# Performance work log

Hardware: AMD Instinct MI355X
Metric: run time of the kernel (lower is better)

The kernel has to match this reference:

```python
import jax, jax.numpy as jnp
import numpy as np

H = 8      # n_heads
DK = 64    # d_k per head
EPS = 1e-5       # InstanceNorm1d eps
SLOPE = 0.01     # LeakyReLU negative slope


def setup_inputs() -> dict:
    key = jax.random.key(0)
    ks = jax.random.split(key, 6)
    B, C, L = 16, 256, 1024
    HD = H * DK  # 512
    return {
        "x": jax.random.normal(ks[0], (B, C, L), dtype=jnp.float32),
        "Wq": jax.random.normal(ks[1], (HD, C), dtype=jnp.float32) * 0.02,
        "Wk": jax.random.normal(ks[2], (HD, C), dtype=jnp.float32) * 0.02,
        "Wv": jax.random.normal(ks[3], (HD, C), dtype=jnp.float32) * 0.02,
        "Wo": jax.random.normal(ks[4], (C, HD), dtype=jnp.float32) * 0.02,
        "gamma": jax.random.normal(ks[5], (1,), dtype=jnp.float32),
    }


def reference(x, Wq, Wk, Wv, Wo, gamma):
    B, C, L = x.shape
    # conv1x1 projections (bias=False) == channel matmuls -> [B, H*DK, L]
    # then reshape/permute into heads: [B, H, L, DK]
    def proj(W):
        y = jnp.einsum('oc,bcl->bol', W, x)          # [B, H*DK, L]
        return y.reshape(B, H, DK, L).transpose(0, 1, 3, 2)  # [B, H, L, DK]

    q, k, v = proj(Wq), proj(Wk), proj(Wv)
    # softmax-free linear attention: (Q K^T / d_k) V
    logits = jnp.einsum('bhld,bhmd->bhlm', q, k) / DK  # [B, H, L, L]
    out = jnp.einsum('bhlm,bhmd->bhld', logits, v)     # [B, H, L, DK]
    # merge heads back to channel-first [B, H*DK, L]
    merged = out.transpose(0, 1, 3, 2).reshape(B, H * DK, L)
    # output conv1x1 -> [B, C, L]
    o = jnp.einsum('oc,bcl->bol', Wo, merged)
    # InstanceNorm1d (affine=False): normalize over L per (b, c)
    mu = jnp.mean(o, axis=-1, keepdims=True)
    var = jnp.var(o, axis=-1, keepdims=True)
    o = (o - mu) * jax.lax.rsqrt(var + EPS)
    # gamma-scaled residual + LeakyReLU
    y = o * gamma + x
    return jnp.where(y >= 0, y, SLOPE * y)
```

## Files before the change

### kernel.cpp

```cpp
#include <hip/hip_runtime.h>

typedef __bf16 bf16;
typedef bf16 bf16x8 __attribute__((ext_vector_type(8)));
typedef bf16 bf16x4 __attribute__((ext_vector_type(4)));
typedef float f32x4 __attribute__((ext_vector_type(4)));

#define EPS 1e-5f
#define SLOPE 0.01f

__device__ __forceinline__ void gld_lds16(const bf16* g, bf16* l) {
    __builtin_amdgcn_global_load_lds(
        (const __attribute__((address_space(1))) unsigned int*)g,
        (__attribute__((address_space(3))) unsigned int*)l, 16, 0, 0);
}

__global__ __launch_bounds__(256) void prep_kernel(
    const float* __restrict__ x,
    const float* __restrict__ Wq, const float* __restrict__ Wk,
    const float* __restrict__ Wv, const float* __restrict__ Wo,
    bf16* __restrict__ xT, bf16* __restrict__ xB,
    bf16* __restrict__ WkB, bf16* __restrict__ WvB,
    bf16* __restrict__ WoB, bf16* __restrict__ WqT)
{
    __shared__ float tile[64][65];
    const int id = blockIdx.x;
    const int t = threadIdx.x;
    if (id < 1024) {
        const int lt = id & 15, ct = (id >> 4) & 3, b = id >> 6;
        {
            const int cl = t >> 2;
            const int l4 = (t & 3) << 4;
            const float* src = x + (size_t)(b * 256 + ct * 64 + cl) * 1024 + lt * 64 + l4;
            float4 v0 = ((const float4*)src)[0];
            float4 v1 = ((const float4*)src)[1];
            float4 v2 = ((const float4*)src)[2];
            float4 v3 = ((const float4*)src)[3];
            bf16x8 r0, r1;
            r0[0]=(bf16)v0.x; r0[1]=(bf16)v0.y; r0[2]=(bf16)v0.z; r0[3]=(bf16)v0.w;
            r0[4]=(bf16)v1.x; r0[5]=(bf16)v1.y; r0[6]=(bf16)v1.z; r0[7]=(bf16)v1.w;
            r1[0]=(bf16)v2.x; r1[1]=(bf16)v2.y; r1[2]=(bf16)v2.z; r1[3]=(bf16)v2.w;
            r1[4]=(bf16)v3.x; r1[5]=(bf16)v3.y; r1[6]=(bf16)v3.z; r1[7]=(bf16)v3.w;
            bf16* xbd = xB + (size_t)(b * 256 + ct * 64 + cl) * 1024 + lt * 64 + l4;
            *(bf16x8*)xbd = r0;
            *(bf16x8*)(xbd + 8) = r1;
            float* tr = &tile[cl][l4];
            tr[0]=v0.x; tr[1]=v0.y; tr[2]=v0.z; tr[3]=v0.w;
            tr[4]=v1.x; tr[5]=v1.y; tr[6]=v1.z; tr[7]=v1.w;
            tr[8]=v2.x; tr[9]=v2.y; tr[10]=v2.z; tr[11]=v2.w;
            tr[12]=v3.x; tr[13]=v3.y; tr[14]=v3.z; tr[15]=v3.w;
        }
        __syncthreads();
        {
            const int lw = t >> 2;
            const int ec = (t & 3) << 4;
            bf16x8 o0, o1;
            #pragma unroll
            for (int ii = 0; ii < 8; ++ii) {
                o0[ii] = (bf16)tile[ec + ii][lw];
                o1[ii] = (bf16)tile[ec + 8 + ii][lw];
            }
            bf16* dst = xT + (size_t)(b * 1024 + lt * 64 + lw) * 256 + ct * 64 + ec;
            *(bf16x8*)dst = o0;
            *(bf16x8*)(dst + 8) = o1;
        }
    } else if (id < 1408) {
        const int i = (id - 1024) * 1024 + t * 4;
        const float* src; bf16* dst;
        if (i < 131072)      { src = Wk + i;            dst = WkB + i; }
        else if (i < 262144) { src = Wv + (i - 131072); dst = WvB + (i - 131072); }
        else                 { src = Wo + (i - 262144); dst = WoB + (i - 262144); }
        float4 v = *(const float4*)src;
        bf16x4 o;
        o[0]=(bf16)v.x; o[1]=(bf16)v.y; o[2]=(bf16)v.z; o[3]=(bf16)v.w;
        *(bf16x4*)dst = o;
    } else {
        const int id2 = id - 1408;
        const int h = id2 >> 2, ct = id2 & 3;
        {
            const int e  = t >> 2;
            const int c4 = (t & 3) << 4;
            const float* src = Wq + (size_t)(h * 64 + e) * 256 + ct * 64 + c4;
            float4 v0 = ((const float4*)src)[0];
            float4 v1 = ((const float4*)src)[1];
            float4 v2 = ((const float4*)src)[2];
            float4 v3 = ((const float4*)src)[3];
            float* tr = &tile[e][c4];
            tr[0]=v0.x; tr[1]=v0.y; tr[2]=v0.z; tr[3]=v0.w;
            tr[4]=v1.x; tr[5]=v1.y; tr[6]=v1.z; tr[7]=v1.w;
            tr[8]=v2.x; tr[9]=v2.y; tr[10]=v2.z; tr[11]=v2.w;
            tr[12]=v3.x; tr[13]=v3.y; tr[14]=v3.z; tr[15]=v3.w;
        }
        __syncthreads();
        {
            const int c  = t >> 2;
            const int e4 = (t & 3) << 4;
            bf16x8 o0, o1;
            #pragma unroll
            for (int ii = 0; ii < 8; ++ii) {
                o0[ii] = (bf16)tile[e4 + ii][c];
                o1[ii] = (bf16)tile[e4 + 8 + ii][c];
            }
            bf16* dst = WqT + (size_t)h * 16384 + (size_t)(ct * 64 + c) * 64 + e4;
            *(bf16x8*)dst = o0;
            *(bf16x8*)(dst + 8) = o1;
        }
    }
}

template<int KDIM, typename OutT>
__global__ __launch_bounds__(256) void gemm128_bt(
    const bf16* __restrict__ A, const bf16* __restrict__ Bt, OutT* __restrict__ C,
    long long sA, long long sBt, long long sC, int ldC)
{
    __shared__ bf16 As[128 * 32];
    __shared__ bf16 Bs[128 * 32];
    const int z = blockIdx.z;
    A  += (size_t)z * sA;
    Bt += (size_t)z * sBt;
    C  += (size_t)z * sC;
    const int m0 = blockIdx.x * 128;
    const int n0 = blockIdx.y * 128;
    const int t = threadIdx.x, w = t >> 6, l = t & 63;
    const int srow = w * 16 + (l >> 2);
    const int ske  = (l & 3) * 8;
    const bf16* ga = A  + (size_t)(m0 + srow) * KDIM + ske;
    const bf16* gb = Bt + (size_t)(n0 + srow) * KDIM + ske;
    bf16* la = As + srow * 32 + ske;
    bf16* lb = Bs + srow * 32 + ske;
    const int lm = l & 15, lq = l >> 4;
    const int wm = (w & 1) * 64, wn = (w >> 1) * 64;

    f32x4 acc[4][4] = {};
    for (int kt = 0; kt < KDIM / 32; ++kt) {
        const int k0 = kt * 32;
        gld_lds16(ga + k0, la);
        gld_lds16(ga + k0 + (size_t)64 * KDIM, la + 64 * 32);
        gld_lds16(gb + k0, lb);
        gld_lds16(gb + k0 + (size_t)64 * KDIM, lb + 64 * 32);
        __syncthreads();
        bf16x8 af[4], bfr[4];
        #pragma unroll
        for (int i = 0; i < 4; ++i)
            af[i] = *(const bf16x8*)(As + (wm + i * 16 + lm) * 32 + lq * 8);
        #pragma unroll
        for (int j = 0; j < 4; ++j)
            bfr[j] = *(const bf16x8*)(Bs + (wn + j * 16 + lm) * 32 + lq * 8);
        #pragma unroll
        for (int i = 0; i < 4; ++i)
            #pragma unroll
            for (int j = 0; j < 4; ++j)
                acc[i][j] = __builtin_amdgcn_mfma_f32_16x16x32_bf16(af[i], bfr[j], acc[i][j], 0, 0, 0);
        __syncthreads();
    }
    #pragma unroll
    for (int i = 0; i < 4; ++i)
        #pragma unroll
        for (int j = 0; j < 4; ++j) {
            const int row = m0 + wm + i * 16 + lq * 4;
            const int col = n0 + wn + j * 16 + lm;
            OutT* cp = C + (size_t)row * ldC + col;
            #pragma unroll
            for (int r = 0; r < 4; ++r)
                cp[(size_t)r * ldC] = (OutT)acc[i][j][r];
        }
}

__global__ __launch_bounds__(256) void chain_kernel(
    const bf16* __restrict__ G, const bf16* __restrict__ WvB,
    const bf16* __restrict__ WkB, const bf16* __restrict__ WqT,
    bf16* __restrict__ WmT)
{
    __shared__ __align__(16) bf16 bufA[64 * 256];
    __shared__ __align__(16) bf16 bufB[256 * 64];
    __shared__ __align__(16) bf16 Ss[64 * 256];
    __shared__ __align__(16) bf16 Tb[64 * 64];

    const int bh = blockIdx.x;
    const int b = bh >> 3, h = bh & 7;
    const int t = threadIdx.x, w = t >> 6, l = t & 63;
    const int lm = l & 15, lq = l >> 4;

    #pragma unroll
    for (int it = 0; it < 8; ++it) {
        const int slot = it * 256 + t;
        const int d = slot >> 5, seg = slot & 31;
        const int kq = (seg & 24) | ((seg & 7) ^ (d & 7));
        gld_lds16(WvB + (size_t)(h * 64 + d) * 256 + kq * 8, bufA + slot * 8);
    }
    f32x4 accS[4][4] = {};
    for (int ck = 0; ck < 4; ++ck) {
        #pragma unroll
        for (int it = 0; it < 8; ++it) {
            const int slot = it * 256 + t;
            const int cp = slot >> 3, seg = slot & 7;
            const int kq = seg ^ (cp & 7);
            gld_lds16(G + (size_t)b * 65536 + (size_t)cp * 256 + ck * 64 + kq * 8,
                      bufB + slot * 8);
        }
        __syncthreads();
        #pragma unroll
        for (int kt = 0; kt < 2; ++kt) {
            bf16x8 af[4], bfr[4];
            #pragma unroll
            for (int mf = 0; mf < 4; ++mf) {
                const int m = mf * 16 + lm;
                const int kqg = ck * 8 + kt * 4 + lq;
                const int seg = (kqg & 24) | ((kqg & 7) ^ (m & 7));
                af[mf] = *(const bf16x8*)(bufA + m * 256 + seg * 8);
            }
            #pragma unroll
            for (int nf = 0; nf < 4; ++nf) {
                const int n = w * 64 + nf * 16 + lm;
                const int kq = kt * 4 + lq;
                const int seg = kq ^ (n & 7);
                bfr[nf] = *(const bf16x8*)(bufB + n * 64 + seg * 8);
            }
            #pragma unroll
            for (int mf = 0; mf < 4; ++mf)
                #pragma unroll
                for (int nf = 0; nf < 4; ++nf)
                    accS[mf][nf] = __builtin_amdgcn_mfma_f32_16x16x32_bf16(
                        af[mf], bfr[nf], accS[mf][nf], 0, 0, 0);
        }
        __syncthreads();
    }
    #pragma unroll
    for (int mf = 0; mf < 4; ++mf)
        #pragma unroll
        for (int nf = 0; nf < 4; ++nf)
            #pragma unroll
            for (int r = 0; r < 4; ++r) {
                const int d = mf * 16 + lq * 4 + r;
                const int cp = w * 64 + nf * 16 + lm;
                const int s32 = cp >> 3;
                const int s = (s32 & 24) | ((s32 & 7) ^ (d & 7));
                Ss[d * 256 + s * 8 + (cp & 7)] = (bf16)accS[mf][nf][r];
            }
    #pragma unroll
    for (int it = 0; it < 8; ++it) {
        const int slot = it * 256 + t;
        const int e = slot >> 5, seg = slot & 31;
        const int kq = (seg & 24) | ((seg & 7) ^ (e & 7));
        gld_lds16(WkB + (size_t)(h * 64 + e) * 256 + kq * 8, bufB + slot * 8);
    }
    __syncthreads();

    const int mh = (w & 1) * 32, nh = (w >> 1) * 32;
    f32x4 accT[2][2] = {};
    #pragma unroll
    for (int kt = 0; kt < 8; ++kt) {
        bf16x8 af[2], bfr[2];
        #pragma unroll
        for (int mf = 0; mf < 2; ++mf) {
            const int m = mh + mf * 16 + lm;
            const int kqg = kt * 4 + lq;
            const int seg = (kqg & 24) | ((kqg & 7) ^ (m & 7));
            af[mf] = *(const bf16x8*)(Ss + m * 256 + seg * 8);
        }
        #pragma unroll
        for (int nf = 0; nf < 2; ++nf) {
            const int n = nh + nf * 16 + lm;
            const int kqg = kt * 4 + lq;
            const int seg = (kqg & 24) | ((kqg & 7) ^ (n & 7));
            bfr[nf] = *(const bf16x8*)(bufB + n * 256 + seg * 8);
        }
        #pragma unroll
        for (int mf = 0; mf < 2; ++mf)
            #pragma unroll
            for (int nf = 0; nf < 2; ++nf)
                accT[mf][nf] = __builtin_amdgcn_mfma_f32_16x16x32_bf16(
                    af[mf], bfr[nf], accT[mf][nf], 0, 0, 0);
    }
    __syncthreads();
    #pragma unroll
    for (int mf = 0; mf < 2; ++mf)
        #pragma unroll
        for (int nf = 0; nf < 2; ++nf)
            #pragma unroll
            for (int r = 0; r < 4; ++r) {
                const int d = mh + mf * 16 + lq * 4 + r;
                const int e = nh + nf * 16 + lm;
                const int seg = (e >> 3) ^ (d & 7);
                Tb[d * 64 + seg * 8 + (e & 7)] = (bf16)(accT[mf][nf][r] * 0.015625f);
            }
    #pragma unroll
    for (int it = 0; it < 8; ++it) {
        const int slot = it * 256 + t;
        const int c = slot >> 3, seg = slot & 7;
        const int kq = seg ^ (c & 7);
        gld_lds16(WqT + (size_t)h * 16384 + (size_t)c * 64 + kq * 8, bufA + slot * 8);
    }
    __syncthreads();

    f32x4 accM[4][4] = {};
    #pragma unroll
    for (int kt = 0; kt < 2; ++kt) {
        const int kq = kt * 4 + lq;
        bf16x8 bfr[4];
        #pragma unroll
        for (int nf = 0; nf < 4; ++nf) {
            const int n = nf * 16 + lm;
            bfr[nf] = *(const bf16x8*)(Tb + n * 64 + (kq ^ (n & 7)) * 8);
        }
        #pragma unroll
        for (int mf = 0; mf < 4; ++mf) {
            const int m = w * 64 + mf * 16 + lm;
            bf16x8 a = *(const bf16x8*)(bufA + m * 64 + (kq ^ (m & 7)) * 8);
            #pragma unroll
            for (int nf = 0; nf < 4; ++nf)
                accM[mf][nf] = __builtin_amdgcn_mfma_f32_16x16x32_bf16(
                    a, bfr[nf], accM[mf][nf], 0, 0, 0);
        }
    }
    bf16* Wg = WmT + (size_t)b * 131072 + h * 64;
    #pragma unroll
    for (int mf = 0; mf < 4; ++mf)
        #pragma unroll
        for (int nf = 0; nf < 4; ++nf)
            #pragma unroll
            for (int r = 0; r < 4; ++r) {
                const int c = w * 64 + mf * 16 + lq * 4 + r;
                const int d = nf * 16 + lm;
                Wg[(size_t)c * 512 + d] = (bf16)accM[mf][nf][r];
            }
}

__global__ __launch_bounds__(256) void outnorm_kernel(
    const bf16* __restrict__ WoB, const bf16* __restrict__ WmT,
    const bf16* __restrict__ xT, const bf16* __restrict__ xB,
    const float* __restrict__ gamma, float* __restrict__ y)
{
    __shared__ __align__(16) bf16 chunkBuf[32768];
    __shared__ __align__(16) bf16 WoS[16 * 512];
    __shared__ __align__(16) bf16 WtS[16 * 256];
    __shared__ float redS[4][16], redQ[4][16], bmu[16], binv[16];

    const int b = blockIdx.x >> 4, ct = blockIdx.x & 15;
    const int c0 = ct * 16;
    const int t = threadIdx.x, w = t >> 6, l = t & 63;
    const int lm = l & 15, lq = l >> 4;

    #pragma unroll
    for (int it = 0; it < 4; ++it) {
        const int slot = it * 256 + t;
        const int co = slot >> 6, seg = slot & 63;
        const int kq = (seg & 56) | ((seg & 7) ^ (co & 7));
        gld_lds16(WoB + (size_t)(c0 + co) * 512 + kq * 8, WoS + slot * 8);
    }
    f32x4 acc1[4] = {};
    for (int ck = 0; ck < 8; ++ck) {
        const int k0 = ck * 64;
        #pragma unroll
        for (int it = 0; it < 8; ++it) {
            const int slot = it * 256 + t;
            const int ci = slot >> 3, seg = slot & 7;
            const int kq = seg ^ (ci & 7);
            gld_lds16(WmT + (size_t)b * 131072 + (size_t)ci * 512 + k0 + kq * 8,
                      chunkBuf + slot * 8);
        }
        __syncthreads();
        #pragma unroll
        for (int kt = 0; kt < 2; ++kt) {
            const int kqg = ck * 8 + kt * 4 + lq;
            const int sa = (kqg & 56) | ((kqg & 7) ^ (lm & 7));
            bf16x8 a = *(const bf16x8*)(WoS + lm * 512 + sa * 8);
            #pragma unroll
            for (int nf = 0; nf < 4; ++nf) {
                const int n = w * 64 + nf * 16 + lm;
                const int kq = kt * 4 + lq;
                bf16x8 bb = *(const bf16x8*)(chunkBuf + n * 64 + (kq ^ (n & 7)) * 8);
                acc1[nf] = __builtin_amdgcn_mfma_f32_16x16x32_bf16(a, bb, acc1[nf], 0, 0, 0);
            }
        }
        __syncthreads();
    }
    #pragma unroll
    for (int nf = 0; nf < 4; ++nf)
        #pragma unroll
        for (int r = 0; r < 4; ++r) {
            const int co = lq * 4 + r;
            const int ci = w * 64 + nf * 16 + lm;
            const int s32 = ci >> 3;
            const int s = (s32 & 24) | ((s32 & 7) ^ (co & 7));
            WtS[co * 256 + s * 8 + (ci & 7)] = (bf16)acc1[nf][r];
        }
    __syncthreads();

    f32x4 acc2[16] = {};
    for (int ck = 0; ck < 8; ++ck) {
        const int k0 = ck * 32;
        #pragma unroll
        for (int it = 0; it < 16; ++it) {
            const int slot = it * 256 + t;
            const int ln = slot >> 2, seg = slot & 3;
            const int kq = seg ^ (ln & 3);
            gld_lds16(xT + (size_t)b * 262144 + (size_t)ln * 256 + k0 + kq * 8,
                      chunkBuf + slot * 8);
        }
        __syncthreads();
        const int kqg = ck * 4 + lq;
        const int sa = (kqg & 24) | ((kqg & 7) ^ (lm & 7));
        bf16x8 a = *(const bf16x8*)(WtS + lm * 256 + sa * 8);
        #pragma unroll
        for (int j = 0; j < 16; ++j) {
            const int n = w * 256 + j * 16 + lm;
            bf16x8 bb = *(const bf16x8*)(chunkBuf + n * 32 + ((lq ^ (n & 3)) * 8));
            acc2[j] = __builtin_amdgcn_mfma_f32_16x16x32_bf16(a, bb, acc2[j], 0, 0, 0);
        }
        __syncthreads();
    }

    float s[4] = {}, q[4] = {};
    #pragma unroll
    for (int j = 0; j < 16; ++j)
        #pragma unroll
        for (int r = 0; r < 4; ++r) {
            const float v = acc2[j][r];
            s[r] += v; q[r] += v * v;
        }
    #pragma unroll
    for (int off = 1; off < 16; off <<= 1)
        #pragma unroll
        for (int r = 0; r < 4; ++r) {
            s[r] += __shfl_xor(s[r], off);
            q[r] += __shfl_xor(q[r], off);
        }
    if (lm == 0)
        #pragma unroll
        for (int r = 0; r < 4; ++r) {
            redS[w][lq * 4 + r] = s[r];
            redQ[w][lq * 4 + r] = q[r];
        }
    __syncthreads();
    if (t < 16) {
        float S = redS[0][t] + redS[1][t] + redS[2][t] + redS[3][t];
        float Q = redQ[0][t] + redQ[1][t] + redQ[2][t] + redQ[3][t];
        const float mu = S * (1.0f / 1024.0f);
        const float var = Q * (1.0f / 1024.0f) - mu * mu;
        bmu[t] = mu;
        binv[t] = rsqrtf(var + EPS);
    }
    bf16* otile = chunkBuf;
    #pragma unroll
    for (int j = 0; j < 16; ++j)
        #pragma unroll
        for (int r = 0; r < 4; ++r)
            otile[(lq * 4 + r) * 1032 + w * 256 + j * 16 + lm] = (bf16)acc2[j][r];
    __syncthreads();

    const float g = gamma[0];
    const int qd = t >> 6, l64 = t & 63;
    #pragma unroll
    for (int i = 0; i < 4; ++i) {
        const int c = qd * 4 + i;
        const float mu = bmu[c], inv = binv[c];
        bf16x8 o0 = *(const bf16x8*)(otile + c * 1032 + l64 * 16);
        bf16x8 o1 = *(const bf16x8*)(otile + c * 1032 + l64 * 16 + 8);
        const bf16* xr = xB + (size_t)(b * 256 + c0 + c) * 1024 + l64 * 16;
        bf16x8 x0 = *(const bf16x8*)xr;
        bf16x8 x1 = *(const bf16x8*)(xr + 8);
        float* yp = y + (size_t)(b * 256 + c0 + c) * 1024 + l64 * 16;
        float4 out[4];
        #pragma unroll
        for (int kk = 0; kk < 8; ++kk) {
            float v0 = ((float)o0[kk] - mu) * inv * g + (float)x0[kk];
            float v1 = ((float)o1[kk] - mu) * inv * g + (float)x1[kk];
            v0 = v0 >= 0.f ? v0 : SLOPE * v0;
            v1 = v1 >= 0.f ? v1 : SLOPE * v1;
            ((float*)out)[kk] = v0;
            ((float*)out)[8 + kk] = v1;
        }
        ((float4*)yp)[0] = out[0];
        ((float4*)yp)[1] = out[1];
        ((float4*)yp)[2] = out[2];
        ((float4*)yp)[3] = out[3];
    }
}

extern "C" void kernel_launch(void* const* d_in, const int* in_sizes, int n_in,
                              void* d_out, int out_size, void* d_ws, size_t ws_size,
                              hipStream_t stream) {
    const float* x     = (const float*)d_in[0];
    const float* Wq    = (const float*)d_in[1];
    const float* Wk    = (const float*)d_in[2];
    const float* Wv    = (const float*)d_in[3];
    const float* Wo    = (const float*)d_in[4];
    const float* gamma = (const float*)d_in[5];
    float* y = (float*)d_out;

    char* wsb = (char*)d_ws;
    bf16* xT  = (bf16*)(wsb);
    bf16* xB  = (bf16*)(wsb +  8388608);
    bf16* WkB = (bf16*)(wsb + 16777216);
    bf16* WvB = (bf16*)(wsb + 17039360);
    bf16* WoB = (bf16*)(wsb + 17301504);
    bf16* WqT = (bf16*)(wsb + 17563648);
    bf16* G   = (bf16*)(wsb + 17825792);
    bf16* WmT = (bf16*)(wsb + 19922944);

    prep_kernel<<<dim3(1440), 256, 0, stream>>>(x, Wq, Wk, Wv, Wo, xT, xB, WkB, WvB, WoB, WqT);

    gemm128_bt<1024, bf16><<<dim3(2, 2, 16), 256, 0, stream>>>(
        xB, xB, G, 262144LL, 262144LL, 65536LL, 256);

    chain_kernel<<<dim3(128), 256, 0, stream>>>(G, WvB, WkB, WqT, WmT);

    outnorm_kernel<<<dim3(256), 256, 0, stream>>>(WoB, WmT, xT, xB, gamma, y);
}
```

Baseline: 140.2 us.

## Fuse four kernel launches into one cooperative kernel with grid syncs

```diff
diff --git a/kernel.cpp b/kernel.cpp
--- a/kernel.cpp
+++ b/kernel.cpp
@@ -1,4 +1,7 @@
 #include <hip/hip_runtime.h>
+#include <hip/hip_cooperative_groups.h>
+
+namespace cg = cooperative_groups;
 
 typedef __bf16 bf16;
 typedef bf16 bf16x8 __attribute__((ext_vector_type(8)));
@@ -14,466 +17,463 @@
         (__attribute__((address_space(3))) unsigned int*)l, 16, 0, 0);
 }
 
-__global__ __launch_bounds__(256) void prep_kernel(
+__global__ __launch_bounds__(256) void fused_kernel(
     const float* __restrict__ x,
     const float* __restrict__ Wq, const float* __restrict__ Wk,
     const float* __restrict__ Wv, const float* __restrict__ Wo,
+    const float* __restrict__ gamma,
     bf16* __restrict__ xT, bf16* __restrict__ xB,
     bf16* __restrict__ WkB, bf16* __restrict__ WvB,
-    bf16* __restrict__ WoB, bf16* __restrict__ WqT)
+    bf16* __restrict__ WoB, bf16* __restrict__ WqT,
+    bf16* __restrict__ Gm, bf16* __restrict__ WmT,
+    float* __restrict__ y)
 {
-    __shared__ float tile[64][65];
-    const int id = blockIdx.x;
+    __shared__ __align__(16) char smem[106496];
+    cg::grid_group grid = cg::this_grid();
+    const int bid = blockIdx.x;
     const int t = threadIdx.x;
-    if (id < 1024) {
-        const int lt = id & 15, ct = (id >> 4) & 3, b = id >> 6;
-        {
-            const int cl = t >> 2;
-            const int l4 = (t & 3) << 4;
-            const float* src = x + (size_t)(b * 256 + ct * 64 + cl) * 1024 + lt * 64 + l4;
-            float4 v0 = ((const float4*)src)[0];
-            float4 v1 = ((const float4*)src)[1];
-            float4 v2 = ((const float4*)src)[2];
-            float4 v3 = ((const float4*)src)[3];
-            bf16x8 r0, r1;
-            r0[0]=(bf16)v0.x; r0[1]=(bf16)v0.y; r0[2]=(bf16)v0.z; r0[3]=(bf16)v0.w;
-            r0[4]=(bf16)v1.x; r0[5]=(bf16)v1.y; r0[6]=(bf16)v1.z; r0[7]=(bf16)v1.w;
-            r1[0]=(bf16)v2.x; r1[1]=(bf16)v2.y; r1[2]=(bf16)v2.z; r1[3]=(bf16)v2.w;
-            r1[4]=(bf16)v3.x; r1[5]=(bf16)v3.y; r1[6]=(bf16)v3.z; r1[7]=(bf16)v3.w;
-            bf16* xbd = xB + (size_t)(b * 256 + ct * 64 + cl) * 1024 + lt * 64 + l4;
-            *(bf16x8*)xbd = r0;
-            *(bf16x8*)(xbd + 8) = r1;
-            float* tr = &tile[cl][l4];
-            tr[0]=v0.x; tr[1]=v0.y; tr[2]=v0.z; tr[3]=v0.w;
-            tr[4]=v1.x; tr[5]=v1.y; tr[6]=v1.z; tr[7]=v1.w;
-            tr[8]=v2.x; tr[9]=v2.y; tr[10]=v2.z; tr[11]=v2.w;
-            tr[12]=v3.x; tr[13]=v3.y; tr[14]=v3.z; tr[15]=v3.w;
-        }
-        __syncthreads();
-        {
-            const int lw = t >> 2;
-            const int ec = (t & 3) << 4;
-            bf16x8 o0, o1;
-            #pragma unroll
-            for (int ii = 0; ii < 8; ++ii) {
-                o0[ii] = (bf16)tile[ec + ii][lw];
-                o1[ii] = (bf16)tile[ec + 8 + ii][lw];
-            }
-            bf16* dst = xT + (size_t)(b * 1024 + lt * 64 + lw) * 256 + ct * 64 + ec;
-            *(bf16x8*)dst = o0;
-            *(bf16x8*)(dst + 8) = o1;
-        }
-    } else if (id < 1408) {
-        const int i = (id - 1024) * 1024 + t * 4;
-        const float* src; bf16* dst;
-        if (i < 131072)      { src = Wk + i;            dst = WkB + i; }
-        else if (i < 262144) { src = Wv + (i - 131072); dst = WvB + (i - 131072); }
-        else                 { src = Wo + (i - 262144); dst = WoB + (i - 262144); }
-        float4 v = *(const float4*)src;
-        bf16x4 o;
-        o[0]=(bf16)v.x; o[1]=(bf16)v.y; o[2]=(bf16)v.z; o[3]=(bf16)v.w;
-        *(bf16x4*)dst = o;
-    } else {
-        const int id2 = id - 1408;
-        const int h = id2 >> 2, ct = id2 & 3;
-        {
-            const int e  = t >> 2;
-            const int c4 = (t & 3) << 4;
-            const float* src = Wq + (size_t)(h * 64 + e) * 256 + ct * 64 + c4;
-            float4 v0 = ((const float4*)src)[0];
-            float4 v1 = ((const float4*)src)[1];
-            float4 v2 = ((const float4*)src)[2];
-            float4 v3 = ((const float4*)src)[3];
-            float* tr = &tile[e][c4];
-            tr[0]=v0.x; tr[1]=v0.y; tr[2]=v0.z; tr[3]=v0.w;
-            tr[4]=v1.x; tr[5]=v1.y; tr[6]=v1.z; tr[7]=v1.w;
-            tr[8]=v2.x; tr[9]=v2.y; tr[10]=v2.z; tr[11]=v2.w;
-            tr[12]=v3.x; tr[13]=v3.y; tr[14]=v3.z; tr[15]=v3.w;
-        }
-        __syncthreads();
-        {
-            const int c  = t >> 2;
-            const int e4 = (t & 3) << 4;
-            bf16x8 o0, o1;
-            #pragma unroll
-            for (int ii = 0; ii < 8; ++ii) {
-                o0[ii] = (bf16)tile[e4 + ii][c];
-                o1[ii] = (bf16)tile[e4 + 8 + ii][c];
-            }
-            bf16* dst = WqT + (size_t)h * 16384 + (size_t)(ct * 64 + c) * 64 + e4;
-            *(bf16x8*)dst = o0;
-            *(bf16x8*)(dst + 8) = o1;
+    const int w = t >> 6, l = t & 63;
+    const int lm = l & 15, lq = l >> 4;
+
+    {
+        float (*tile)[65] = (float(*)[65])smem;
+        for (int id = bid; id < 1440; id += 256) {
+            if (id < 1024) {
+                const int lt = id & 15, ct = (id >> 4) & 3, b = id >> 6;
+                {
+                    const int cl = t >> 2;
+                    const int l4 = (t & 3) << 4;
+                    const float* src = x + (size_t)(b * 256 + ct * 64 + cl) * 1024 + lt * 64 + l4;
+                    float4 v0 = ((const float4*)src)[0];
+                    float4 v1 = ((const float4*)src)[1];
+                    float4 v2 = ((const float4*)src)[2];
+                    float4 v3 = ((const float4*)src)[3];
+                    bf16x8 r0, r1;
+                    r0[0]=(bf16)v0.x; r0[1]=(bf16)v0.y; r0[2]=(bf16)v0.z; r0[3]=(bf16)v0.w;
+                    r0[4]=(bf16)v1.x; r0[5]=(bf16)v1.y; r0[6]=(bf16)v1.z; r0[7]=(bf16)v1.w;
+                    r1[0]=(bf16)v2.x; r1[1]=(bf16)v2.y; r1[2]=(bf16)v2.z; r1[3]=(bf16)v2.w;
+                    r1[4]=(bf16)v3.x; r1[5]=(bf16)v3.y; r1[6]=(bf16)v3.z; r1[7]=(bf16)v3.w;
+                    bf16* xbd = xB + (size_t)(b * 256 + ct * 64 + cl) * 1024 + lt * 64 + l4;
+                    *(bf16x8*)xbd = r0;
+                    *(bf16x8*)(xbd + 8) = r1;
+                    float* tr = &tile[cl][l4];
+                    tr[0]=v0.x; tr[1]=v0.y; tr[2]=v0.z; tr[3]=v0.w;
+                    tr[4]=v1.x; tr[5]=v1.y; tr[6]=v1.z; tr[7]=v1.w;
+                    tr[8]=v2.x; tr[9]=v2.y; tr[10]=v2.z; tr[11]=v2.w;
+                    tr[12]=v3.x; tr[13]=v3.y; tr[14]=v3.z; tr[15]=v3.w;
+                }
+                __syncthreads();
+                {
+                    const int lw = t >> 2;
+                    const int ec = (t & 3) << 4;
+                    bf16x8 o0, o1;
+                    #pragma unroll
+                    for (int ii = 0; ii < 8; ++ii) {
+                        o0[ii] = (bf16)tile[ec + ii][lw];
+                        o1[ii] = (bf16)tile[ec + 8 + ii][lw];
+                    }
+                    bf16* dst = xT + (size_t)(b * 1024 + lt * 64 + lw) * 256 + ct * 64 + ec;
+                    *(bf16x8*)dst = o0;
+                    *(bf16x8*)(dst + 8) = o1;
+                }
+            } else if (id < 1408) {
+                const int i = (id - 1024) * 1024 + t * 4;
+                const float* src; bf16* dst;
+                if (i < 131072)      { src = Wk + i;            dst = WkB + i; }
+                else if (i < 262144) { src = Wv + (i - 131072); dst = WvB + (i - 131072); }
+                else                 { src = Wo + (i - 262144); dst = WoB + (i - 262144); }
+                float4 v = *(const float4*)src;
+                bf16x4 o;
+                o[0]=(bf16)v.x; o[1]=(bf16)v.y; o[2]=(bf16)v.z; o[3]=(bf16)v.w;
+                *(bf16x4*)dst = o;
+            } else {
+                const int id2 = id - 1408;
+                const int h = id2 >> 2, ct = id2 & 3;
+                {
+                    const int e  = t >> 2;
+                    const int c4 = (t & 3) << 4;
+                    const float* src = Wq + (size_t)(h * 64 + e) * 256 + ct * 64 + c4;
+                    float4 v0 = ((const float4*)src)[0];
+                    float4 v1 = ((const float4*)src)[1];
+                    float4 v2 = ((const float4*)src)[2];
+                    float4 v3 = ((const float4*)src)[3];
+                    float* tr = &tile[e][c4];
+                    tr[0]=v0.x; tr[1]=v0.y; tr[2]=v0.z; tr[3]=v0.w;
+                    tr[4]=v1.x; tr[5]=v1.y; tr[6]=v1.z; tr[7]=v1.w;
+                    tr[8]=v2.x; tr[9]=v2.y; tr[10]=v2.z; tr[11]=v2.w;
+                    tr[12]=v3.x; tr[13]=v3.y; tr[14]=v3.z; tr[15]=v3.w;
+                }
+                __syncthreads();
+                {
+                    const int c  = t >> 2;
+                    const int e4 = (t & 3) << 4;
+                    bf16x8 o0, o1;
+                    #pragma unroll
+                    for (int ii = 0; ii < 8; ++ii) {
+                        o0[ii] = (bf16)tile[e4 + ii][c];
+                        o1[ii] = (bf16)tile[e4 + 8 + ii][c];
+                    }
+                    bf16* dst = WqT + (size_t)h * 16384 + (size_t)(ct * 64 + c) * 64 + e4;
+                    *(bf16x8*)dst = o0;
+                    *(bf16x8*)(dst + 8) = o1;
+                }
+            }
+            __syncthreads();
         }
     }
-}
-
-template<int KDIM, typename OutT>
-__global__ __launch_bounds__(256) void gemm128_bt(
-    const bf16* __restrict__ A, const bf16* __restrict__ Bt, OutT* __restrict__ C,
-    long long sA, long long sBt, long long sC, int ldC)
-{
-    __shared__ bf16 As[128 * 32];
-    __shared__ bf16 Bs[128 * 32];
-    const int z = blockIdx.z;
-    A  += (size_t)z * sA;
-    Bt += (size_t)z * sBt;
-    C  += (size_t)z * sC;
-    const int m0 = blockIdx.x * 128;
-    const int n0 = blockIdx.y * 128;
-    const int t = threadIdx.x, w = t >> 6, l = t & 63;
-    const int srow = w * 16 + (l >> 2);
-    const int ske  = (l & 3) * 8;
-    const bf16* ga = A  + (size_t)(m0 + srow) * KDIM + ske;
-    const bf16* gb = Bt + (size_t)(n0 + srow) * KDIM + ske;
-    bf16* la = As + srow * 32 + ske;
-    bf16* lb = Bs + srow * 32 + ske;
-    const int lm = l & 15, lq = l >> 4;
-    const int wm = (w & 1) * 64, wn = (w >> 1) * 64;
-
-    f32x4 acc[4][4] = {};
-    for (int kt = 0; kt < KDIM / 32; ++kt) {
-        const int k0 = kt * 32;
-        gld_lds16(ga + k0, la);
-        gld_lds16(ga + k0 + (size_t)64 * KDIM, la + 64 * 32);
-        gld_lds16(gb + k0, lb);
-        gld_lds16(gb + k0 + (size_t)64 * KDIM, lb + 64 * 32);
-        __syncthreads();
-        bf16x8 af[4], bfr[4];
+    grid.sync();
+
+    if (bid < 64) {
+        bf16* As = (bf16*)smem;
+        bf16* Bs = (bf16*)(smem + 8192);
+        const int z = bid >> 2;
+        const int m0 = (bid & 1) * 128;
+        const int n0 = ((bid >> 1) & 1) * 128;
+        const bf16* Ab = xB + (size_t)z * 262144;
+        const int srow = w * 16 + (l >> 2);
+        const int ske  = (l & 3) * 8;
+        const bf16* ga = Ab + (size_t)(m0 + srow) * 1024 + ske;
+        const bf16* gb = Ab + (size_t)(n0 + srow) * 1024 + ske;
+        bf16* la = As + srow * 32 + ske;
+        bf16* lb = Bs + srow * 32 + ske;
+        const int wm = (w & 1) * 64, wn = (w >> 1) * 64;
+
+        f32x4 acc[4][4] = {};
+        for (int kt = 0; kt < 32; ++kt) {
+            const int k0 = kt * 32;
+            gld_lds16(ga + k0, la);
+            gld_lds16(ga + k0 + (size_t)64 * 1024, la + 64 * 32);
+            gld_lds16(gb + k0, lb);
+            gld_lds16(gb + k0 + (size_t)64 * 1024, lb + 64 * 32);
+            __syncthreads();
+            bf16x8 af[4], bfr[4];
+            #pragma unroll
+            for (int i = 0; i < 4; ++i)
+                af[i] = *(const bf16x8*)(As + (wm + i * 16 + lm) * 32 + lq * 8);
+            #pragma unroll
+            for (int j = 0; j < 4; ++j)
+                bfr[j] = *(const bf16x8*)(Bs + (wn + j * 16 + lm) * 32 + lq * 8);
+            #pragma unroll
+            for (int i = 0; i < 4; ++i)
+                #pragma unroll
+                for (int j = 0; j < 4; ++j)
+                    acc[i][j] = __builtin_amdgcn_mfma_f32_16x16x32_bf16(af[i], bfr[j], acc[i][j], 0, 0, 0);
+            __syncthreads();
+        }
         #pragma unroll
         for (int i = 0; i < 4; ++i)
-            af[i] = *(const bf16x8*)(As + (wm + i * 16 + lm) * 32 + lq * 8);
-        #pragma unroll
-        for (int j = 0; j < 4; ++j)
-            bfr[j] = *(const bf16x8*)(Bs + (wn + j * 16 + lm) * 32 + lq * 8);
-        #pragma unroll
-        for (int i = 0; i < 4; ++i)
-            #pragma unroll
-            for (int j = 0; j < 4; ++j)
-                acc[i][j] = __builtin_amdgcn_mfma_f32_16x16x32_bf16(af[i], bfr[j], acc[i][j], 0, 0, 0);
-        __syncthreads();
+            #pragma unroll
+            for (int j = 0; j < 4; ++j) {
+                const int row = m0 + wm + i * 16 + lq * 4;
+                const int col = n0 + wn + j * 16 + lm;
+                bf16* cp = Gm + (size_t)z * 65536 + (size_t)row * 256 + col;
+                #pragma unroll
+                for (int r = 0; r < 4; ++r)
+                    cp[(size_t)r * 256] = (bf16)acc[i][j][r];
+            }
     }
-    #pragma unroll
-    for (int i = 0; i < 4; ++i)
-        #pragma unroll
-        for (int j = 0; j < 4; ++j) {
-            const int row = m0 + wm + i * 16 + lq * 4;
-            const int col = n0 + wn + j * 16 + lm;
-            OutT* cp = C + (size_t)row * ldC + col;
-            #pragma unroll
-            for (int r = 0; r < 4; ++r)
-                cp[(size_t)r * ldC] = (OutT)acc[i][j][r];
-        }
-}
-
-__global__ __launch_bounds__(256) void chain_kernel(
-    const bf16* __restrict__ G, const bf16* __restrict__ WvB,
-    const bf16* __restrict__ WkB, const bf16* __restrict__ WqT,
-    bf16* __restrict__ WmT)
-{
-    __shared__ __align__(16) bf16 bufA[64 * 256];
-    __shared__ __align__(16) bf16 bufB[256 * 64];
-    __shared__ __align__(16) bf16 Ss[64 * 256];
-    __shared__ __align__(16) bf16 Tb[64 * 64];
-
-    const int bh = blockIdx.x;
-    const int b = bh >> 3, h = bh & 7;
-    const int t = threadIdx.x, w = t >> 6, l = t & 63;
-    const int lm = l & 15, lq = l >> 4;
-
-    #pragma unroll
-    for (int it = 0; it < 8; ++it) {
-        const int slot = it * 256 + t;
-        const int d = slot >> 5, seg = slot & 31;
-        const int kq = (seg & 24) | ((seg & 7) ^ (d & 7));
-        gld_lds16(WvB + (size_t)(h * 64 + d) * 256 + kq * 8, bufA + slot * 8);
-    }
-    f32x4 accS[4][4] = {};
-    for (int ck = 0; ck < 4; ++ck) {
+    grid.sync();
+
+    if (bid < 128) {
+        bf16* bufA = (bf16*)smem;
+        bf16* bufB = (bf16*)(smem + 32768);
+        bf16* Ss   = (bf16*)(smem + 65536);
+        bf16* Tb   = (bf16*)(smem + 98304);
+        const int b = bid >> 3, h = bid & 7;
+
         #pragma unroll
         for (int it = 0; it < 8; ++it) {
             const int slot = it * 256 + t;
-            const int cp = slot >> 3, seg = slot & 7;
-            const int kq = seg ^ (cp & 7);
-            gld_lds16(G + (size_t)b * 65536 + (size_t)cp * 256 + ck * 64 + kq * 8,
-                      bufB + slot * 8);
-        }
-        __syncthreads();
-        #pragma unroll
-        for (int kt = 0; kt < 2; ++kt) {
-            bf16x8 af[4], bfr[4];
-            #pragma unroll
-            for (int mf = 0; mf < 4; ++mf) {
-                const int m = mf * 16 + lm;
-                const int kqg = ck * 8 + kt * 4 + lq;
-                const int seg = (kqg & 24) | ((kqg & 7) ^ (m & 7));
-                af[mf] = *(const bf16x8*)(bufA + m * 256 + seg * 8);
-            }
-            #pragma unroll
-            for (int nf = 0; nf < 4; ++nf) {
-                const int n = w * 64 + nf * 16 + lm;
-                const int kq = kt * 4 + lq;
-                const int seg = kq ^ (n & 7);
-                bfr[nf] = *(const bf16x8*)(bufB + n * 64 + seg * 8);
-            }
-            #pragma unroll
-            for (int mf = 0; mf < 4; ++mf)
-                #pragma unroll
-                for (int nf = 0; nf < 4; ++nf)
-                    accS[mf][nf] = __builtin_amdgcn_mfma_f32_16x16x32_bf16(
-                        af[mf], bfr[nf], accS[mf][nf], 0, 0, 0);
-        }
-        __syncthreads();
-    }
-    #pragma unroll
-    for (int mf = 0; mf < 4; ++mf)
-        #pragma unroll
-        for (int nf = 0; nf < 4; ++nf)
-            #pragma unroll
-            for (int r = 0; r < 4; ++r) {
-                const int d = mf * 16 + lq * 4 + r;
-                const int cp = w * 64 + nf * 16 + lm;
-                const int s32 = cp >> 3;
-                const int s = (s32 & 24) | ((s32 & 7) ^ (d & 7));
-                Ss[d * 256 + s * 8 + (cp & 7)] = (bf16)accS[mf][nf][r];
-            }
-    #pragma unroll
-    for (int it = 0; it < 8; ++it) {
-        const int slot = it * 256 + t;
-        const int e = slot >> 5, seg = slot & 31;
-        const int kq = (seg & 24) | ((seg & 7) ^ (e & 7));
-        gld_lds16(WkB + (size_t)(h * 64 + e) * 256 + kq * 8, bufB + slot * 8);
-    }
-    __syncthreads();
-
-    const int mh = (w & 1) * 32, nh = (w >> 1) * 32;
-    f32x4 accT[2][2] = {};
-    #pragma unroll
-    for (int kt = 0; kt < 8; ++kt) {
-        bf16x8 af[2], bfr[2];
-        #pragma unroll
-        for (int mf = 0; mf < 2; ++mf) {
-            const int m = mh + mf * 16 + lm;
-            const int kqg = kt * 4 + lq;
-            const int seg = (kqg & 24) | ((kqg & 7) ^ (m & 7));
-            af[mf] = *(const bf16x8*)(Ss + m * 256 + seg * 8);
-        }
-        #pragma unroll
-        for (int nf = 0; nf < 2; ++nf) {
-            const int n = nh + nf * 16 + lm;
-            const int kqg = kt * 4 + lq;
-            const int seg = (kqg & 24) | ((kqg & 7) ^ (n & 7));
-            bfr[nf] = *(const bf16x8*)(bufB + n * 256 + seg * 8);
-        }
-        #pragma unroll
-        for (int mf = 0; mf < 2; ++mf)
-            #pragma unroll
-            for (int nf = 0; nf < 2; ++nf)
-                accT[mf][nf] = __builtin_amdgcn_mfma_f32_16x16x32_bf16(
-                    af[mf], bfr[nf], accT[mf][nf], 0, 0, 0);
-    }
-    __syncthreads();
-    #pragma unroll
-    for (int mf = 0; mf < 2; ++mf)
-        #pragma unroll
-        for (int nf = 0; nf < 2; ++nf)
-            #pragma unroll
-            for (int r = 0; r < 4; ++r) {
-                const int d = mh + mf * 16 + lq * 4 + r;
-                const int e = nh + nf * 16 + lm;
-                const int seg = (e >> 3) ^ (d & 7);
-                Tb[d * 64 + seg * 8 + (e & 7)] = (bf16)(accT[mf][nf][r] * 0.015625f);
-            }
-    #pragma unroll
-    for (int it = 0; it < 8; ++it) {
-        const int slot = it * 256 + t;
-        const int c = slot >> 3, seg = slot & 7;
-        const int kq = seg ^ (c & 7);
-        gld_lds16(WqT + (size_t)h * 16384 + (size_t)c * 64 + kq * 8, bufA + slot * 8);
-    }
-    __syncthreads();
-
-    f32x4 accM[4][4] = {};
-    #pragma unroll
-    for (int kt = 0; kt < 2; ++kt) {
-        const int kq = kt * 4 + lq;
-        bf16x8 bfr[4];
-        #pragma unroll
-        for (int nf = 0; nf < 4; ++nf) {
-            const int n = nf * 16 + lm;
-            bfr[nf] = *(const bf16x8*)(Tb + n * 64 + (kq ^ (n & 7)) * 8);
-        }
-        #pragma unroll
-        for (int mf = 0; mf < 4; ++mf) {
-            const int m = w * 64 + mf * 16 + lm;
-            bf16x8 a = *(const bf16x8*)(bufA + m * 64 + (kq ^ (m & 7)) * 8);
+            const int d = slot >> 5, seg = slot & 31;
+            const int kq = (seg & 24) | ((seg & 7) ^ (d & 7));
+            gld_lds16(WvB + (size_t)(h * 64 + d) * 256 + kq * 8, bufA + slot * 8);
+        }
+        f32x4 accS[4][4] = {};
+        for (int ck = 0; ck < 4; ++ck) {
+            #pragma unroll
+            for (int it = 0; it < 8; ++it) {
+                const int slot = it * 256 + t;
+                const int cp = slot >> 3, seg = slot & 7;
+                const int kq = seg ^ (cp & 7);
+                gld_lds16(Gm + (size_t)b * 65536 + (size_t)cp * 256 + ck * 64 + kq * 8,
+                          bufB + slot * 8);
+            }
+            __syncthreads();
+            #pragma unroll
+            for (int kt = 0; kt < 2; ++kt) {
+                bf16x8 af[4], bfr[4];
+                #pragma unroll
+                for (int mf = 0; mf < 4; ++mf) {
+                    const int m = mf * 16 + lm;
+                    const int kqg = ck * 8 + kt * 4 + lq;
+                    const int seg = (kqg & 24) | ((kqg & 7) ^ (m & 7));
+                    af[mf] = *(const bf16x8*)(bufA + m * 256 + seg * 8);
+                }
+                #pragma unroll
+                for (int nf = 0; nf < 4; ++nf) {
+                    const int n = w * 64 + nf * 16 + lm;
+                    const int kq = kt * 4 + lq;
+                    const int seg = kq ^ (n & 7);
+                    bfr[nf] = *(const bf16x8*)(bufB + n * 64 + seg * 8);
+                }
+                #pragma unroll
+                for (int mf = 0; mf < 4; ++mf)
+                    #pragma unroll
+                    for (int nf = 0; nf < 4; ++nf)
+                        accS[mf][nf] = __builtin_amdgcn_mfma_f32_16x16x32_bf16(
+                            af[mf], bfr[nf], accS[mf][nf], 0, 0, 0);
+            }
+            __syncthreads();
+        }
+        #pragma unroll
+        for (int mf = 0; mf < 4; ++mf)
             #pragma unroll
             for (int nf = 0; nf < 4; ++nf)
-                accM[mf][nf] = __builtin_amdgcn_mfma_f32_16x16x32_bf16(
-                    a, bfr[nf], accM[mf][nf], 0, 0, 0);
-        }
-    }
-    bf16* Wg = WmT + (size_t)b * 131072 + h * 64;
-    #pragma unroll
-    for (int mf = 0; mf < 4; ++mf)
-        #pragma unroll
-        for (int nf = 0; nf < 4; ++nf)
-            #pragma unroll
-            for (int r = 0; r < 4; ++r) {
-                const int c = w * 64 + mf * 16 + lq * 4 + r;
-                const int d = nf * 16 + lm;
-                Wg[(size_t)c * 512 + d] = (bf16)accM[mf][nf][r];
-            }
-}
-
-__global__ __launch_bounds__(256) void outnorm_kernel(
-    const bf16* __restrict__ WoB, const bf16* __restrict__ WmT,
-    const bf16* __restrict__ xT, const bf16* __restrict__ xB,
-    const float* __restrict__ gamma, float* __restrict__ y)
-{
-    __shared__ __align__(16) bf16 chunkBuf[32768];
-    __shared__ __align__(16) bf16 WoS[16 * 512];
-    __shared__ __align__(16) bf16 WtS[16 * 256];
-    __shared__ float redS[4][16], redQ[4][16], bmu[16], binv[16];
-
-    const int b = blockIdx.x >> 4, ct = blockIdx.x & 15;
-    const int c0 = ct * 16;
-    const int t = threadIdx.x, w = t >> 6, l = t & 63;
-    const int lm = l & 15, lq = l >> 4;
-
-    #pragma unroll
-    for (int it = 0; it < 4; ++it) {
-        const int slot = it * 256 + t;
-        const int co = slot >> 6, seg = slot & 63;
-        const int kq = (seg & 56) | ((seg & 7) ^ (co & 7));
-        gld_lds16(WoB + (size_t)(c0 + co) * 512 + kq * 8, WoS + slot * 8);
-    }
-    f32x4 acc1[4] = {};
-    for (int ck = 0; ck < 8; ++ck) {
-        const int k0 = ck * 64;
+                #pragma unroll
+                for (int r = 0; r < 4; ++r) {
+                    const int d = mf * 16 + lq * 4 + r;
+                    const int cp = w * 64 + nf * 16 + lm;
+                    const int s32 = cp >> 3;
+                    const int s = (s32 & 24) | ((s32 & 7) ^ (d & 7));
+                    Ss[d * 256 + s * 8 + (cp & 7)] = (bf16)accS[mf][nf][r];
+                }
         #pragma unroll
         for (int it = 0; it < 8; ++it) {
             const int slot = it * 256 + t;
-            const int ci = slot >> 3, seg = slot & 7;
-            const int kq = seg ^ (ci & 7);
-            gld_lds16(WmT + (size_t)b * 131072 + (size_t)ci * 512 + k0 + kq * 8,
-                      chunkBuf + slot * 8);
+            const int e = slot >> 5, seg = slot & 31;
+            const int kq = (seg & 24) | ((seg & 7) ^ (e & 7));
+            gld_lds16(WkB + (size_t)(h * 64 + e) * 256 + kq * 8, bufB + slot * 8);
         }
         __syncthreads();
+
+        const int mh = (w & 1) * 32, nh = (w >> 1) * 32;
+        f32x4 accT[2][2] = {};
+        #pragma unroll
+        for (int kt = 0; kt < 8; ++kt) {
+            bf16x8 af[2], bfr[2];
+            #pragma unroll
+            for (int mf = 0; mf < 2; ++mf) {
+                const int m = mh + mf * 16 + lm;
+                const int kqg = kt * 4 + lq;
+                const int seg = (kqg & 24) | ((kqg & 7) ^ (m & 7));
+                af[mf] = *(const bf16x8*)(Ss + m * 256 + seg * 8);
+            }
+            #pragma unroll
+            for (int nf = 0; nf < 2; ++nf) {
+                const int n = nh + nf * 16 + lm;
+                const int kqg = kt * 4 + lq;
+                const int seg = (kqg & 24) | ((kqg & 7) ^ (n & 7));
+                bfr[nf] = *(const bf16x8*)(bufB + n * 256 + seg * 8);
+            }
+            #pragma unroll
+            for (int mf = 0; mf < 2; ++mf)
+                #pragma unroll
+                for (int nf = 0; nf < 2; ++nf)
+                    accT[mf][nf] = __builtin_amdgcn_mfma_f32_16x16x32_bf16(
+                        af[mf], bfr[nf], accT[mf][nf], 0, 0, 0);
+        }
+        __syncthreads();
+        #pragma unroll
+        for (int mf = 0; mf < 2; ++mf)
+            #pragma unroll
+            for (int nf = 0; nf < 2; ++nf)
+                #pragma unroll
+                for (int r = 0; r < 4; ++r) {
+                    const int d = mh + mf * 16 + lq * 4 + r;
+                    const int e = nh + nf * 16 + lm;
+                    const int seg = (e >> 3) ^ (d & 7);
+                    Tb[d * 64 + seg * 8 + (e & 7)] = (bf16)(accT[mf][nf][r] * 0.015625f);
+                }
+        #pragma unroll
+        for (int it = 0; it < 8; ++it) {
+            const int slot = it * 256 + t;
+            const int c = slot >> 3, seg = slot & 7;
+            const int kq = seg ^ (c & 7);
+            gld_lds16(WqT + (size_t)h * 16384 + (size_t)c * 64 + kq * 8, bufA + slot * 8);
+        }
+        __syncthreads();
+
+        f32x4 accM[4][4] = {};
         #pragma unroll
         for (int kt = 0; kt < 2; ++kt) {
-            const int kqg = ck * 8 + kt * 4 + lq;
-            const int sa = (kqg & 56) | ((kqg & 7) ^ (lm & 7));
-            bf16x8 a = *(const bf16x8*)(WoS + lm * 512 + sa * 8);
+            const int kq = kt * 4 + lq;
+            bf16x8 bfr[4];
             #pragma unroll
             for (int nf = 0; nf < 4; ++nf) {
-                const int n = w * 64 + nf * 16 + lm;
-                const int kq = kt * 4 + lq;
-                bf16x8 bb = *(const bf16x8*)(chunkBuf + n * 64 + (kq ^ (n & 7)) * 8);
-                acc1[nf] = __builtin_amdgcn_mfma_f32_16x16x32_bf16(a, bb, acc1[nf], 0, 0, 0);
-            }
-        }
+                const int n = nf * 16 + lm;
+                bfr[nf] = *(const bf16x8*)(Tb + n * 64 + (kq ^ (n & 7)) * 8);
+            }
+            #pragma unroll
+            for (int mf = 0; mf < 4; ++mf) {
+                const int m = w * 64 + mf * 16 + lm;
+                bf16x8 a = *(const bf16x8*)(bufA + m * 64 + (kq ^ (m & 7)) * 8);
+                #pragma unroll
+                for (int nf = 0; nf < 4; ++nf)
+                    accM[mf][nf] = __builtin_amdgcn_mfma_f32_16x16x32_bf16(
+                        a, bfr[nf], accM[mf][nf], 0, 0, 0);
+            }
+        }
+        bf16* Wg = WmT + (size_t)b * 131072 + h * 64;
+        #pragma unroll
+        for (int mf = 0; mf < 4; ++mf)
+            #pragma unroll
+            for (int nf = 0; nf < 4; ++nf)
+                #pragma unroll
+                for (int r = 0; r < 4; ++r) {
+                    const int c = w * 64 + mf * 16 + lq * 4 + r;
+                    const int d = nf * 16 + lm;
+                    Wg[(size_t)c * 512 + d] = (bf16)accM[mf][nf][r];
+                }
+    }
+    grid.sync();
+
+    {
+        bf16* chunkBuf = (bf16*)smem;
+        bf16* WoS      = (bf16*)(smem + 65536);
+        bf16* WtS      = (bf16*)(smem + 81920);
+        float* redS    = (float*)(smem + 90112);
+        float* redQ    = (float*)(smem + 90368);
+        float* bmu     = (float*)(smem + 90624);
+        float* binv    = (float*)(smem + 90688);
+
+        const int b = bid >> 4, ct = bid & 15;
+        const int c0 = ct * 16;
+
+        #pragma unroll
+        for (int it = 0; it < 4; ++it) {
+            const int slot = it * 256 + t;
+            const int co = slot >> 6, seg = slot & 63;
+            const int kq = (seg & 56) | ((seg & 7) ^ (co & 7));
+            gld_lds16(WoB + (size_t)(c0 + co) * 512 + kq * 8, WoS + slot * 8);
+        }
+        f32x4 acc1[4] = {};
+        for (int ck = 0; ck < 8; ++ck) {
+            const int k0 = ck * 64;
+            #pragma unroll
+            for (int it = 0; it < 8; ++it) {
+                const int slot = it * 256 + t;
+                const int ci = slot >> 3, seg = slot & 7;
+                const int kq = seg ^ (ci & 7);
+                gld_lds16(WmT + (size_t)b * 131072 + (size_t)ci * 512 + k0 + kq * 8,
+                          chunkBuf + slot * 8);
+            }
+            __syncthreads();
+            #pragma unroll
+            for (int kt = 0; kt < 2; ++kt) {
+                const int kqg = ck * 8 + kt * 4 + lq;
+                const int sa = (kqg & 56) | ((kqg & 7) ^ (lm & 7));
+                bf16x8 a = *(const bf16x8*)(WoS + lm * 512 + sa * 8);
+                #pragma unroll
+                for (int nf = 0; nf < 4; ++nf) {
+                    const int n = w * 64 + nf * 16 + lm;
+                    const int kq = kt * 4 + lq;
+                    bf16x8 bb = *(const bf16x8*)(chunkBuf + n * 64 + (kq ^ (n & 7)) * 8);
+                    acc1[nf] = __builtin_amdgcn_mfma_f32_16x16x32_bf16(a, bb, acc1[nf], 0, 0, 0);
+                }
+            }
+            __syncthreads();
+        }
+        #pragma unroll
+        for (int nf = 0; nf < 4; ++nf)
+            #pragma unroll
+            for (int r = 0; r < 4; ++r) {
+                const int co = lq * 4 + r;
+                const int ci = w * 64 + nf * 16 + lm;
+                const int s32 = ci >> 3;
+                const int s = (s32 & 24) | ((s32 & 7) ^ (co & 7));
+                WtS[co * 256 + s * 8 + (ci & 7)] = (bf16)acc1[nf][r];
+            }
         __syncthreads();
-    }
-    #pragma unroll
-    for (int nf = 0; nf < 4; ++nf)
-        #pragma unroll
-        for (int r = 0; r < 4; ++r) {
-            const int co = lq * 4 + r;
-            const int ci = w * 64 + nf * 16 + lm;
-            const int s32 = ci >> 3;
-            const int s = (s32 & 24) | ((s32 & 7) ^ (co & 7));
-            WtS[co * 256 + s * 8 + (ci & 7)] = (bf16)acc1[nf][r];
-        }
-    __syncthreads();
-
-    f32x4 acc2[16] = {};
-    for (int ck = 0; ck < 8; ++ck) {
-        const int k0 = ck * 32;
-        #pragma unroll
-        for (int it = 0; it < 16; ++it) {
-            const int slot = it * 256 + t;
-            const int ln = slot >> 2, seg = slot & 3;
-            const int kq = seg ^ (ln & 3);
-            gld_lds16(xT + (size_t)b * 262144 + (size_t)ln * 256 + k0 + kq * 8,
-                      chunkBuf + slot * 8);
-        }
+
+        f32x4 acc2[16] = {};
+        for (int ck = 0; ck < 8; ++ck) {
+            const int k0 = ck * 32;
+            #pragma unroll
+            for (int it = 0; it < 16; ++it) {
+                const int slot = it * 256 + t;
+                const int ln = slot >> 2, seg = slot & 3;
+                const int kq = seg ^ (ln & 3);
+                gld_lds16(xT + (size_t)b * 262144 + (size_t)ln * 256 + k0 + kq * 8,
+                          chunkBuf + slot * 8);
+            }
+            __syncthreads();
+            const int kqg = ck * 4 + lq;
+            const int sa = (kqg & 24) | ((kqg & 7) ^ (lm & 7));
+            bf16x8 a = *(const bf16x8*)(WtS + lm * 256 + sa * 8);
+            #pragma unroll
+            for (int j = 0; j < 16; ++j) {
+                const int n = w * 256 + j * 16 + lm;
+                bf16x8 bb = *(const bf16x8*)(chunkBuf + n * 32 + ((lq ^ (n & 3)) * 8));
+                acc2[j] = __builtin_amdgcn_mfma_f32_16x16x32_bf16(a, bb, acc2[j], 0, 0, 0);
+            }
+            __syncthreads();
+        }
+
+        float s[4] = {}, q[4] = {};
+        #pragma unroll
+        for (int j = 0; j < 16; ++j)
+            #pragma unroll
+            for (int r = 0; r < 4; ++r) {
+                const float v = acc2[j][r];
+                s[r] += v; q[r] += v * v;
+            }
+        #pragma unroll
+        for (int off = 1; off < 16; off <<= 1)
+            #pragma unroll
+            for (int r = 0; r < 4; ++r) {
+                s[r] += __shfl_xor(s[r], off);
+                q[r] += __shfl_xor(q[r], off);
+            }
+        if (lm == 0)
+            #pragma unroll
+            for (int r = 0; r < 4; ++r) {
+                redS[w * 16 + lq * 4 + r] = s[r];
+                redQ[w * 16 + lq * 4 + r] = q[r];
+            }
         __syncthreads();
-        const int kqg = ck * 4 + lq;
-        const int sa = (kqg & 24) | ((kqg & 7) ^ (lm & 7));
-        bf16x8 a = *(const bf16x8*)(WtS + lm * 256 + sa * 8);
-        #pragma unroll
-        for (int j = 0; j < 16; ++j) {
-            const int n = w * 256 + j * 16 + lm;
-            bf16x8 bb = *(const bf16x8*)(chunkBuf + n * 32 + ((lq ^ (n & 3)) * 8));
-            acc2[j] = __builtin_amdgcn_mfma_f32_16x16x32_bf16(a, bb, acc2[j], 0, 0, 0);
-        }
+        if (t < 16) {
+            float S = redS[t] + redS[16 + t] + redS[32 + t] + redS[48 + t];
+            float Q = redQ[t] + redQ[16 + t] + redQ[32 + t] + redQ[48 + t];
+            const float mu = S * (1.0f / 1024.0f);
+            const float var = Q * (1.0f / 1024.0f) - mu * mu;
+            bmu[t] = mu;
+            binv[t] = rsqrtf(var + EPS);
+        }
+        bf16* otile = chunkBuf;
+        #pragma unroll
+        for (int j = 0; j < 16; ++j)
+            #pragma unroll
+            for (int r = 0; r < 4; ++r)
+                otile[(lq * 4 + r) * 1032 + w * 256 + j * 16 + lm] = (bf16)acc2[j][r];
         __syncthreads();
-    }
-
-    float s[4] = {}, q[4] = {};
-    #pragma unroll
-    for (int j = 0; j < 16; ++j)
-        #pragma unroll
-        for (int r = 0; r < 4; ++r) {
-            const float v = acc2[j][r];
-            s[r] += v; q[r] += v * v;
-        }
-    #pragma unroll
-    for (int off = 1; off < 16; off <<= 1)
-        #pragma unroll
-        for (int r = 0; r < 4; ++r) {
-            s[r] += __shfl_xor(s[r], off);
-            q[r] += __shfl_xor(q[r], off);
-        }
-    if (lm == 0)
-        #pragma unroll
-        for (int r = 0; r < 4; ++r) {
-            redS[w][lq * 4 + r] = s[r];
-            redQ[w][lq * 4 + r] = q[r];
-        }
-    __syncthreads();
-    if (t < 16) {
-        float S = redS[0][t] + redS[1][t] + redS[2][t] + redS[3][t];
-        float Q = redQ[0][t] + redQ[1][t] + redQ[2][t] + redQ[3][t];
-        const float mu = S * (1.0f / 1024.0f);
-        const float var = Q * (1.0f / 1024.0f) - mu * mu;
-        bmu[t] = mu;
-        binv[t] = rsqrtf(var + EPS);
-    }
-    bf16* otile = chunkBuf;
-    #pragma unroll
-    for (int j = 0; j < 16; ++j)
-        #pragma unroll
-        for (int r = 0; r < 4; ++r)
-            otile[(lq * 4 + r) * 1032 + w * 256 + j * 16 + lm] = (bf16)acc2[j][r];
-    __syncthreads();
-
-    const float g = gamma[0];
-    const int qd = t >> 6, l64 = t & 63;
-    #pragma unroll
-    for (int i = 0; i < 4; ++i) {
-        const int c = qd * 4 + i;
-        const float mu = bmu[c], inv = binv[c];
-        bf16x8 o0 = *(const bf16x8*)(otile + c * 1032 + l64 * 16);
-        bf16x8 o1 = *(const bf16x8*)(otile + c * 1032 + l64 * 16 + 8);
-        const bf16* xr = xB + (size_t)(b * 256 + c0 + c) * 1024 + l64 * 16;
-        bf16x8 x0 = *(const bf16x8*)xr;
-        bf16x8 x1 = *(const bf16x8*)(xr + 8);
-        float* yp = y + (size_t)(b * 256 + c0 + c) * 1024 + l64 * 16;
-        float4 out[4];
-        #pragma unroll
-        for (int kk = 0; kk < 8; ++kk) {
-            float v0 = ((float)o0[kk] - mu) * inv * g + (float)x0[kk];
-            float v1 = ((float)o1[kk] - mu) * inv * g + (float)x1[kk];
-            v0 = v0 >= 0.f ? v0 : SLOPE * v0;
-            v1 = v1 >= 0.f ? v1 : SLOPE * v1;
-            ((float*)out)[kk] = v0;
-            ((float*)out)[8 + kk] = v1;
-        }
-        ((float4*)yp)[0] = out[0];
-        ((float4*)yp)[1] = out[1];
-        ((float4*)yp)[2] = out[2];
-        ((float4*)yp)[3] = out[3];
+
+        const float g = gamma[0];
+        const int qd = t >> 6, l64 = t & 63;
+        #pragma unroll
+        for (int i = 0; i < 4; ++i) {
+            const int c = qd * 4 + i;
+            const float mu = bmu[c], inv = binv[c];
+            bf16x8 o0 = *(const bf16x8*)(otile + c * 1032 + l64 * 16);
+            bf16x8 o1 = *(const bf16x8*)(otile + c * 1032 + l64 * 16 + 8);
+            const bf16* xr = xB + (size_t)(b * 256 + c0 + c) * 1024 + l64 * 16;
+            bf16x8 x0 = *(const bf16x8*)xr;
+            bf16x8 x1 = *(const bf16x8*)(xr + 8);
+            float* yp = y + (size_t)(b * 256 + c0 + c) * 1024 + l64 * 16;
+            float4 out[4];
+            #pragma unroll
+            for (int kk = 0; kk < 8; ++kk) {
+                float v0 = ((float)o0[kk] - mu) * inv * g + (float)x0[kk];
+                float v1 = ((float)o1[kk] - mu) * inv * g + (float)x1[kk];
+                v0 = v0 >= 0.f ? v0 : SLOPE * v0;
+                v1 = v1 >= 0.f ? v1 : SLOPE * v1;
+                ((float*)out)[kk] = v0;
+                ((float*)out)[8 + kk] = v1;
+            }
+            ((float4*)yp)[0] = out[0];
+            ((float4*)yp)[1] = out[1];
+            ((float4*)yp)[2] = out[2];
+            ((float4*)yp)[3] = out[3];
+        }
     }
 }
 
@@ -495,15 +495,14 @@
     bf16* WvB = (bf16*)(wsb + 17039360);
     bf16* WoB = (bf16*)(wsb + 17301504);
     bf16* WqT = (bf16*)(wsb + 17563648);
-    bf16* G   = (bf16*)(wsb + 17825792);
+    bf16* Gm  = (bf16*)(wsb + 17825792);
     bf16* WmT = (bf16*)(wsb + 19922944);
 
-    prep_kernel<<<dim3(1440), 256, 0, stream>>>(x, Wq, Wk, Wv, Wo, xT, xB, WkB, WvB, WoB, WqT);
-
-    gemm128_bt<1024, bf16><<<dim3(2, 2, 16), 256, 0, stream>>>(
-        xB, xB, G, 262144LL, 262144LL, 65536LL, 256);
-
-    chain_kernel<<<dim3(128), 256, 0, stream>>>(G, WvB, WkB, WqT, WmT);
-
-    outnorm_kernel<<<dim3(256), 256, 0, stream>>>(WoB, WmT, xT, xB, gamma, y);
+    void* args[] = {
+        (void*)&x, (void*)&Wq, (void*)&Wk, (void*)&Wv, (void*)&Wo, (void*)&gamma,
+        (void*)&xT, (void*)&xB, (void*)&WkB, (void*)&WvB, (void*)&WoB, (void*)&WqT,
+        (void*)&Gm, (void*)&WmT, (void*)&y
+    };
+    hipLaunchCooperativeKernel((void*)fused_kernel, dim3(256), dim3(256),
+                               args, 0, stream);
 }
```

Result: slower. 244.5 us (+74.4%).
